# Performance work log

Measured on AMD Instinct MI355X. Metric: run time of the kernel, lower is better.

## Reference

```python
import jax, jax.numpy as jnp
import numpy as np
from jax import lax

B, S, H, SS, DS = 512, 200, 128, 2, 2  # batch, seq_len, hidden, static_size, dynamic_size

def _xavier(k, shape):
    fan_in, fan_out = shape[-1], shape[0]
    lim = float(np.sqrt(6.0 / (fan_in + fan_out)))
    return jax.random.uniform(k, shape, jnp.float32, -lim, lim)

def setup_inputs() -> dict:
    key = jax.random.key(0)
    ks = jax.random.split(key, 20)
    return {
        "static":  jax.random.uniform(ks[0], (B, SS, S), jnp.float32),
        "dynamic": jax.random.uniform(ks[1], (B, DS, S), jnp.float32),
        # Encoder: 1x1 Conv1d weights stored as [H, C] (kernel dim squeezed)
        "sW": _xavier(ks[2], (H, SS)),  "sb": jnp.zeros((H,), jnp.float32),
        "dW": _xavier(ks[3], (H, DS)),  "db": jnp.zeros((H,), jnp.float32),
        # Decoder learned initial output / hidden
        "x0": _xavier(ks[4], (1, SS)),  "h0": _xavier(ks[5], (1, H)),
        # Decoder input embedding Linear(SS -> H)
        "Wemb": _xavier(ks[6], (H, SS)), "bemb": jnp.zeros((H,), jnp.float32),
        # GRU (1 layer): torch layout [3H, H] gates ordered (r, z, n)
        "Wih": _xavier(ks[7], (3 * H, H)), "Whh": _xavier(ks[8], (3 * H, H)),
        "bih": jnp.zeros((3 * H,), jnp.float32), "bhh": jnp.zeros((3 * H,), jnp.float32),
        # Attention: v [H], W [H, 3H]
        "Wa": _xavier(ks[9], (H, 3 * H)), "va": _xavier(ks[10], (1, H))[0],
        # Decoder pointer head: v [H], W [H, 2H]
        "Wd": _xavier(ks[11], (H, 2 * H)), "vd": _xavier(ks[12], (1, H))[0],
    }

def _decode(static, dynamic, sW, sb, dW, db, x0, h0, Wemb, bemb,
            Wih, Whh, bih, bhh, Wa, va, Wd, vd):
    # Encoder: 1x1 convs == per-node linear maps  -> [B, H, S]
    static_enc  = jnp.einsum('hc,bcs->bhs', sW, static)  + sb[None, :, None]
    dynamic_enc = jnp.einsum('hc,bcs->bhs', dW, dynamic) + db[None, :, None]

    keys = jax.random.split(jax.random.key(42), S)  # one sample key per decode step
    static_sg = lax.stop_gradient(static)           # mirrors static.data gather in torch

    def step(carry, key):
        last_out, h = carry                              # [B,SS], [B,H]
        emb = last_out @ Wemb.T + bemb                   # [B,H]
        # GRU cell (torch gate order r, z, n)
        gi = emb @ Wih.T + bih                           # [B,3H]
        gh = h @ Whh.T + bhh
        r = jax.nn.sigmoid(gi[:, :H] + gh[:, :H])
        z = jax.nn.sigmoid(gi[:, H:2 * H] + gh[:, H:2 * H])
        n = jnp.tanh(gi[:, 2 * H:] + r * gh[:, 2 * H:])
        h_new = (1.0 - z) * n + z * h                    # [B,H]
        # Additive attention over nodes (vectorized over batch)
        hid = jnp.broadcast_to(h_new[:, :, None], (B, H, S))
        energy = jnp.concatenate([static_enc, dynamic_enc, hid], axis=1)   # [B,3H,S]
        attn = jax.nn.softmax(
            jnp.einsum('h,bhs->bs', va, jnp.tanh(jnp.einsum('hk,bks->bhs', Wa, energy))),
            axis=1)                                      # [B,S]
        context = jnp.einsum('bs,bhs->bh', attn, static_enc)               # [B,H]
        ctx = jnp.concatenate(
            [static_enc, jnp.broadcast_to(context[:, :, None], (B, H, S))], axis=1)  # [B,2H,S]
        logits = jnp.einsum('h,bhs->bs', vd,
                            jnp.tanh(jnp.einsum('hk,bks->bhs', Wd, ctx)))  # [B,S]
        # mask is all ones (mask_fn=None) -> log(mask)=0
        probs = jax.nn.softmax(logits, axis=1)
        idx = jax.random.categorical(key, logits, axis=1)                  # [B] int
        next_out = jnp.take_along_axis(static_sg, idx[:, None, None], axis=2)[:, :, 0]  # [B,SS]
        chosen_p = jnp.take_along_axis(probs, idx[:, None], axis=1)[:, 0]  # [B]
        return (next_out, h_new), (idx, chosen_p)

    init = (jnp.broadcast_to(x0, (B, SS)), jnp.broadcast_to(h0, (B, H)))
    _, (idx_seq, prob_seq) = lax.scan(step, init, keys)
    return idx_seq.T, prob_seq.T                          # [B,S] each

def reference(static, dynamic, sW, sb, dW, db, x0, h0, Wemb, bemb,
              Wih, Whh, bih, bhh, Wa, va, Wd, vd):
    return _decode(static, dynamic, sW, sb, dW, db, x0, h0, Wemb, bemb,
                   Wih, Whh, bih, bhh, Wa, va, Wd, vd)
```

## Files before the change

kernel.cpp:

```cpp
#include <hip/hip_runtime.h>
#include <stdint.h>
#include <math.h>

#define NB 512
#define NS 200
#define NH 128
#define NH3 384
#define NT 1024
#define NWAVE 16

#define IDX4(h) ((h) + (((h) >> 6) << 2))
#define IDX1(h) ((h) + (((h) >> 6) << 4))

__device__ __forceinline__ float xla_tanhf(float x) {
  float cx = fminf(fmaxf(x, -9.0f), 9.0f);
  float x2 = __fmul_rn(cx, cx);
  float p = -2.76076847742355e-16f;
  p = __fadd_rn(__fmul_rn(x2, p), 2.00018790482477e-13f);
  p = __fadd_rn(__fmul_rn(x2, p), -8.60467152213735e-11f);
  p = __fadd_rn(__fmul_rn(x2, p), 5.12229709037114e-08f);
  p = __fadd_rn(__fmul_rn(x2, p), 1.48572235717979e-05f);
  p = __fadd_rn(__fmul_rn(x2, p), 6.37261928875436e-04f);
  p = __fadd_rn(__fmul_rn(x2, p), 4.89352455891786e-03f);
  p = __fmul_rn(cx, p);
  float q = 1.19825839466702e-06f;
  q = __fadd_rn(__fmul_rn(x2, q), 1.18534705686654e-04f);
  q = __fadd_rn(__fmul_rn(x2, q), 2.26843463243900e-03f);
  q = __fadd_rn(__fmul_rn(x2, q), 4.89352518554385e-03f);
  float r = __fdiv_rn(p, q);
  return (fabsf(x) < 0.0004f) ? x : r;
}

__device__ __forceinline__ float xla_sigmoidf(float x) {
  return __fadd_rn(0.5f, __fmul_rn(0.5f, xla_tanhf(__fmul_rn(0.5f, x))));
}

__device__ __forceinline__ uint32_t rotl32(uint32_t v, int r) {
  return (v << r) | (v >> (32 - r));
}
__device__ __forceinline__ void threefry2x32(uint32_t k0, uint32_t k1,
                                             uint32_t x0, uint32_t x1,
                                             uint32_t& o0, uint32_t& o1) {
  uint32_t k2 = k0 ^ k1 ^ 0x1BD11BDAu;
  x0 += k0; x1 += k1;
  #define TFR(r) { x0 += x1; x1 = rotl32(x1, r); x1 ^= x0; }
  TFR(13) TFR(15) TFR(26) TFR(6)
  x0 += k1; x1 += k2 + 1u;
  TFR(17) TFR(29) TFR(16) TFR(24)
  x0 += k2; x1 += k0 + 2u;
  TFR(13) TFR(15) TFR(26) TFR(6)
  x0 += k0; x1 += k1 + 3u;
  TFR(17) TFR(29) TFR(16) TFR(24)
  x0 += k1; x1 += k2 + 4u;
  TFR(13) TFR(15) TFR(26) TFR(6)
  x0 += k2; x1 += k0 + 5u;
  #undef TFR
  o0 = x0; o1 = x1;
}

__device__ __forceinline__ float bits_to_gumbel(uint32_t bits) {
  const float kTiny = 1.1754943508222875e-38f;
  float f = __fsub_rn(__uint_as_float((bits >> 9) | 0x3F800000u), 1.0f);
  float u = __fadd_rn(__fmul_rn(f, __fsub_rn(1.0f, kTiny)), kTiny);
  u = fmaxf(kTiny, u);
  return -logf(-logf(u));
}

__global__ __launch_bounds__(NT, 4) void k_decode(
    const float* __restrict__ stat, const float* __restrict__ dyn,
    const float* __restrict__ sW,   const float* __restrict__ sb,
    const float* __restrict__ dW,   const float* __restrict__ db,
    const float* __restrict__ x0,   const float* __restrict__ h0,
    const float* __restrict__ Wemb, const float* __restrict__ bemb,
    const float* __restrict__ Wih,  const float* __restrict__ Whh,
    const float* __restrict__ bih,  const float* __restrict__ bhh,
    const float* __restrict__ Wa,   const float* __restrict__ va,
    const float* __restrict__ Wd,   const float* __restrict__ vd,
    float* __restrict__ out) {

  __shared__ __align__(16) float st0A[NS], st1A[NS], dy0A[NS], dy1A[NS];
  __shared__ __align__(16) float st0B[NS], st1B[NS], dy0B[NS], dy1B[NS];
  __shared__ float4 AF4p[132];
  __shared__ float4 DFSp[132];
  __shared__ float4 CW4[NH];
  __shared__ float  vaP[144];
  __shared__ float  Ht2A[144], Ht2B[144];
  __shared__ float  ct2A[144], ct2B[144];
  __shared__ float  AcL[NH];
  __shared__ float WembL[2*NH], bembL[NH];
  __shared__ float bihL[NH3], bhhL[NH3];
  __shared__ __align__(16) float embA[NH], embB[NH], hA[NH], hB[NH];
  __shared__ float giA[NH3], ghA[NH3], giB[NH3], ghB[NH3];
  __shared__ float ex2A[NS], ex2B[NS], gumA[NS], gumB[NS];
  __shared__ uint32_t keysL[2*NS];
  __shared__ float xpA[2], xpB[2];
  __shared__ float SvL[2];
  __shared__ float part[NWAVE][8];
  __shared__ int   partI[NWAVE];

  const int t = threadIdx.x;
  const int bA = blockIdx.x;
  const int bB = blockIdx.x + 256;
  const int w = t >> 6;
  const bool rB = (t >= 512);
  const int tr = rB ? (t - 512) : t;
  const int s = tr >> 1;
  const int h0i = (tr & 1) * 64;
  const int b4 = h0i + ((h0i >> 6) << 2);
  const int b1 = h0i + ((h0i >> 6) << 4);
  const bool act = (tr < 2*NS);

  if (t < NS) {
    st0A[t] = stat[(size_t)bA*2*NS + t];
    st1A[t] = stat[(size_t)bA*2*NS + NS + t];
    dy0A[t] = dyn[(size_t)bA*2*NS + t];
    dy1A[t] = dyn[(size_t)bA*2*NS + NS + t];
    uint32_t q0, q1;
    threefry2x32(0u, 42u, 0u, (uint32_t)t, q0, q1);
    keysL[2*t] = q0; keysL[2*t + 1] = q1;
  } else if (t >= 256 && t < 256 + NS) {
    int si = t - 256;
    st0B[si] = stat[(size_t)bB*2*NS + si];
    st1B[si] = stat[(size_t)bB*2*NS + NS + si];
    dy0B[si] = dyn[(size_t)bB*2*NS + si];
    dy1B[si] = dyn[(size_t)bB*2*NS + NS + si];
  }
  if (t >= 512 && t < 512 + NH) {
    int h = t - 512;
    const float* war = Wa + (size_t)h * NH3;
    float as0 = 0.f, as1 = 0.f, ad0 = 0.f, ad1 = 0.f, ac = 0.f;
    for (int k = 0; k < NH; ++k) {
      as0 = fmaf(war[k],     sW[k*2+0], as0);
      as1 = fmaf(war[k],     sW[k*2+1], as1);
      ad0 = fmaf(war[NH+k],  dW[k*2+0], ad0);
      ad1 = fmaf(war[NH+k],  dW[k*2+1], ad1);
      ac  = fmaf(war[k],     sb[k],     ac);
    }
    for (int k = 0; k < NH; ++k) ac = fmaf(war[NH+k], db[k], ac);
    AF4p[IDX4(h)] = make_float4(2.f*as0, 2.f*as1, 2.f*ad0, 2.f*ad1);
    vaP[IDX1(h)] = va[h];
    AcL[h] = ac;

    const float* wdr = Wd + (size_t)h * 256;
    float ds0 = 0.f, ds1 = 0.f, dc = 0.f, c0 = 0.f, c1 = 0.f, cb = 0.f;
    for (int k = 0; k < NH; ++k) {
      ds0 = fmaf(wdr[k],    sW[k*2+0], ds0);
      ds1 = fmaf(wdr[k],    sW[k*2+1], ds1);
      dc  = fmaf(wdr[k],    sb[k],     dc);
      c0  = fmaf(wdr[NH+k], sW[k*2+0], c0);
      c1  = fmaf(wdr[NH+k], sW[k*2+1], c1);
      cb  = fmaf(wdr[NH+k], sb[k],     cb);
    }
    DFSp[IDX4(h)] = make_float4(2.f*ds0, 2.f*ds1, vd[h], 0.f);
    CW4[h] = make_float4(2.f*c0, 2.f*c1, 2.f*cb, 2.f*dc);

    bembL[h] = bemb[h];
    WembL[2*h]   = Wemb[2*h];
    WembL[2*h+1] = Wemb[2*h+1];
    hA[h] = h0[h];
    hB[h] = h0[h];
  }
  for (int i = t; i < NH3; i += NT) { bihL[i] = bih[i]; bhhL[i] = bhh[i]; }
  if (t == 0) {
    xpA[0] = x0[0]; xpA[1] = x0[1];
    xpB[0] = x0[0]; xpB[1] = x0[1];
    float sva = 0.f, svd = 0.f;
    for (int h = 0; h < NH; ++h) { sva = __fadd_rn(sva, va[h]); svd = __fadd_rn(svd, vd[h]); }
    SvL[0] = sva; SvL[1] = svd;
  }
  __syncthreads();

  float s0r = 0.f, s1r = 0.f, d0r = 0.f, d1r = 0.f;
  if (act) {
    if (!rB) { s0r = st0A[s]; s1r = st1A[s]; d0r = dy0A[s]; d1r = dy1A[s]; }
    else     { s0r = st0B[s]; s1r = st1B[s]; d0r = dy0B[s]; d1r = dy1B[s]; }
  }
  const float svaR = SvL[0], svdR = SvL[1];
  const float* HtX = rB ? Ht2B : Ht2A;
  const float* ctX = rB ? ct2B : ct2A;
  const float* gumX = rB ? gumB : gumA;

  for (int step = 0; step < NS; ++step) {
    if (t < NH) {
      float e = fmaf(xpA[1], WembL[t*2+1], __fmul_rn(xpA[0], WembL[t*2+0]));
      embA[t] = __fadd_rn(e, bembL[t]);
    } else if (t < 2*NH) {
      int h = t - NH;
      float e = fmaf(xpB[1], WembL[h*2+1], __fmul_rn(xpB[0], WembL[h*2+0]));
      embB[h] = __fadd_rn(e, bembL[h]);
    } else if (t < 2*NH + 2*NS) {
      int gi = t - 2*NH;
      uint32_t k0 = keysL[2*step], k1 = keysL[2*step + 1];
      uint32_t q0, q1;
      if (gi < NS) {
        threefry2x32(k0, k1, 0u, (uint32_t)(bA*NS + gi), q0, q1);
        gumA[gi] = bits_to_gumbel(q0 ^ q1);
      } else {
        int si = gi - NS;
        threefry2x32(k0, k1, 0u, (uint32_t)(bB*NS + si), q0, q1);
        gumB[si] = bits_to_gumbel(q0 ^ q1);
      }
    }
    __syncthreads();

    if (t < 2*NH3) {
      const bool isWih = (t < NH3);
      const float4* wp = isWih
          ? (const float4*)(Wih + (size_t)t * NH)
          : (const float4*)(Whh + (size_t)(t - NH3) * NH);
      const float4* opA = isWih ? (const float4*)embA : (const float4*)hA;
      const float4* opB = isWih ? (const float4*)embB : (const float4*)hB;
      float aA = 0.f, aB = 0.f;
      #pragma unroll 8
      for (int k4 = 0; k4 < 32; ++k4) {
        float4 c = wp[k4];
        float4 vA = opA[k4], vB = opB[k4];
        aA = fmaf(c.x, vA.x, aA); aA = fmaf(c.y, vA.y, aA);
        aA = fmaf(c.z, vA.z, aA); aA = fmaf(c.w, vA.w, aA);
        aB = fmaf(c.x, vB.x, aB); aB = fmaf(c.y, vB.y, aB);
        aB = fmaf(c.z, vB.z, aB); aB = fmaf(c.w, vB.w, aB);
      }
      if (isWih) {
        giA[t] = __fadd_rn(aA, bihL[t]);
        giB[t] = __fadd_rn(aB, bihL[t]);
      } else {
        int row = t - NH3;
        ghA[row] = __fadd_rn(aA, bhhL[row]);
        ghB[row] = __fadd_rn(aB, bhhL[row]);
      }
    }
    __syncthreads();

    if (t < NH) {
      float r = xla_sigmoidf(__fadd_rn(giA[t],      ghA[t]));
      float z = xla_sigmoidf(__fadd_rn(giA[t+NH],   ghA[t+NH]));
      float n = xla_tanhf(__fadd_rn(giA[t+2*NH], __fmul_rn(r, ghA[t+2*NH])));
      float hv = hA[t];
      hA[t] = __fadd_rn(__fmul_rn(__fsub_rn(1.0f, z), n), __fmul_rn(z, hv));
    } else if (t < 2*NH) {
      int h = t - NH;
      float r = xla_sigmoidf(__fadd_rn(giB[h],      ghB[h]));
      float z = xla_sigmoidf(__fadd_rn(giB[h+NH],   ghB[h+NH]));
      float n = xla_tanhf(__fadd_rn(giB[h+2*NH], __fmul_rn(r, ghB[h+2*NH])));
      float hv = hB[h];
      hB[h] = __fadd_rn(__fmul_rn(__fsub_rn(1.0f, z), n), __fmul_rn(z, hv));
    }
    __syncthreads();

    if (t < NH) {
      const float4* war = (const float4*)(Wa + (size_t)t*NH3 + 2*NH);
      const float4* hn4 = (const float4*)hA;
      float acc = 0.f;
      #pragma unroll 8
      for (int k4 = 0; k4 < 32; ++k4) {
        float4 a = war[k4], hv = hn4[k4];
        acc = fmaf(a.x, hv.x, acc); acc = fmaf(a.y, hv.y, acc);
        acc = fmaf(a.z, hv.z, acc); acc = fmaf(a.w, hv.w, acc);
      }
      Ht2A[IDX1(t)] = __fmul_rn(2.0f, __fadd_rn(acc, AcL[t]));
    } else if (t < 2*NH) {
      int h = t - NH;
      const float4* war = (const float4*)(Wa + (size_t)h*NH3 + 2*NH);
      const float4* hn4 = (const float4*)hB;
      float acc = 0.f;
      #pragma unroll 8
      for (int k4 = 0; k4 < 32; ++k4) {
        float4 a = war[k4], hv = hn4[k4];
        acc = fmaf(a.x, hv.x, acc); acc = fmaf(a.y, hv.y, acc);
        acc = fmaf(a.z, hv.z, acc); acc = fmaf(a.w, hv.w, acc);
      }
      Ht2B[IDX1(h)] = __fmul_rn(2.0f, __fadd_rn(acc, AcL[h]));
    }
    __syncthreads();

    float accE = 0.f;
    if (act) {
      #pragma unroll 4
      for (int j = 0; j < 64; ++j) {
        float4 af = AF4p[b4 + j];
        float e2 = fmaf(af.x, s0r, HtX[b1 + j]);
        e2 = fmaf(af.y, s1r, e2);
        e2 = fmaf(af.z, d0r, e2);
        e2 = fmaf(af.w, d1r, e2);
        float r = __builtin_amdgcn_rcpf(__fadd_rn(__expf(e2), 1.0f));
        accE = fmaf(vaP[b1 + j], r, accE);
      }
    }
    float accSum = __fadd_rn(accE, __shfl_xor(accE, 1));
    float sc = act ? fmaf(-2.0f, accSum, svaR) : 0.f;

    float exv = act ? __expf(sc) : 0.f;
    {
      float sm = exv;
      float c0 = __fmul_rn(exv, s0r);
      float c1 = __fmul_rn(exv, s1r);
      #pragma unroll
      for (int mm = 2; mm < 64; mm <<= 1) {
        sm = __fadd_rn(sm, __shfl_xor(sm, mm));
        c0 = __fadd_rn(c0, __shfl_xor(c0, mm));
        c1 = __fadd_rn(c1, __shfl_xor(c1, mm));
      }
      if ((t & 63) == 0) { part[w][0] = sm; part[w][1] = c0; part[w][2] = c1; }
    }
    __syncthreads();

    if (t < 2*NH) {
      int h = t & (NH - 1);
      int base = (t < NH) ? 0 : 8;
      float sume = part[base][0], r0 = part[base][1], r1 = part[base][2];
      #pragma unroll
      for (int ww = 1; ww < 8; ++ww) {
        sume = __fadd_rn(sume, part[base + ww][0]);
        r0   = __fadd_rn(r0,   part[base + ww][1]);
        r1   = __fadd_rn(r1,   part[base + ww][2]);
      }
      r0 = __fdiv_rn(r0, sume); r1 = __fdiv_rn(r1, sume);
      float4 cw = CW4[h];
      float ct2 = fmaf(r0, cw.x, fmaf(r1, cw.y, cw.z));
      if (t < NH) ct2A[IDX1(h)] = __fadd_rn(cw.w, ct2);
      else        ct2B[IDX1(h)] = __fadd_rn(cw.w, ct2);
    }
    __syncthreads();

    float accD = 0.f;
    if (act) {
      #pragma unroll 4
      for (int j = 0; j < 64; ++j) {
        float4 df = DFSp[b4 + j];
        float d2 = fmaf(df.x, s0r, ctX[b1 + j]);
        d2 = fmaf(df.y, s1r, d2);
        float r = __builtin_amdgcn_rcpf(__fadd_rn(__expf(d2), 1.0f));
        accD = fmaf(df.z, r, accD);
      }
    }
    float accDS = __fadd_rn(accD, __shfl_xor(accD, 1));
    float sc2 = act ? fmaf(-2.0f, accDS, svdR) : 0.f;

    float e2v = act ? __expf(sc2) : 0.f;
    if (act && (tr & 1) == 0) { if (!rB) ex2A[s] = e2v; else ex2B[s] = e2v; }
    {
      float gv = -INFINITY;
      int gidx = 1 << 20;
      if (act) {
        gv = __fadd_rn(gumX[s], sc2);
        gidx = s;
      }
      float sm = e2v;
      #pragma unroll
      for (int mm = 2; mm < 64; mm <<= 1) {
        sm = __fadd_rn(sm, __shfl_xor(sm, mm));
        float ov = __shfl_xor(gv, mm); int oi = __shfl_xor(gidx, mm);
        if (ov > gv || (ov == gv && oi < gidx)) { gv = ov; gidx = oi; }
      }
      if ((t & 63) == 0) { part[w][3] = sm; part[w][4] = gv; partI[w] = gidx; }
    }
    __syncthreads();

    if (t == 0) {
      float bv = part[0][4]; int bi = partI[0];
      float sume2 = part[0][3];
      #pragma unroll
      for (int ww = 1; ww < 8; ++ww) {
        float vv = part[ww][4]; int ii = partI[ww];
        if (vv > bv || (vv == bv && ii < bi)) { bv = vv; bi = ii; }
        sume2 = __fadd_rn(sume2, part[ww][3]);
      }
      out[(size_t)bA*NS + step] = (float)bi;
      out[(size_t)NB*NS + (size_t)bA*NS + step] = __fdiv_rn(ex2A[bi], sume2);
      xpA[0] = st0A[bi]; xpA[1] = st1A[bi];
    } else if (t == 512) {
      float bv = part[8][4]; int bi = partI[8];
      float sume2 = part[8][3];
      #pragma unroll
      for (int ww = 9; ww < 16; ++ww) {
        float vv = part[ww][4]; int ii = partI[ww];
        if (vv > bv || (vv == bv && ii < bi)) { bv = vv; bi = ii; }
        sume2 = __fadd_rn(sume2, part[ww][3]);
      }
      out[(size_t)bB*NS + step] = (float)bi;
      out[(size_t)NB*NS + (size_t)bB*NS + step] = __fdiv_rn(ex2B[bi], sume2);
      xpB[0] = st0B[bi]; xpB[1] = st1B[bi];
    }
    __syncthreads();
  }
}

extern "C" void kernel_launch(void* const* d_in, const int* in_sizes, int n_in,
                              void* d_out, int out_size, void* d_ws, size_t ws_size,
                              hipStream_t stream) {
  (void)in_sizes; (void)n_in; (void)out_size; (void)d_ws; (void)ws_size;
  const float* stat = (const float*)d_in[0];
  const float* dyn  = (const float*)d_in[1];
  const float* sW   = (const float*)d_in[2];
  const float* sb   = (const float*)d_in[3];
  const float* dW   = (const float*)d_in[4];
  const float* db   = (const float*)d_in[5];
  const float* x0   = (const float*)d_in[6];
  const float* h0   = (const float*)d_in[7];
  const float* Wemb = (const float*)d_in[8];
  const float* bemb = (const float*)d_in[9];
  const float* Wih  = (const float*)d_in[10];
  const float* Whh  = (const float*)d_in[11];
  const float* bih  = (const float*)d_in[12];
  const float* bhh  = (const float*)d_in[13];
  const float* Wa   = (const float*)d_in[14];
  const float* va   = (const float*)d_in[15];
  const float* Wd   = (const float*)d_in[16];
  const float* vd   = (const float*)d_in[17];
  float* out = (float*)d_out;

  k_decode<<<NB/2, NT, 0, stream>>>(stat, dyn, sW, sb, dW, db, x0, h0,
                                    Wemb, bemb, Wih, Whh, bih, bhh,
                                    Wa, va, Wd, vd, out);
}
```

Baseline: 5.487 ms.

## Fuse embedding and Gumbel prep into step tail, use exp2 with split accumulators

Removes one block-wide barrier per decode step. Each step's tail phase now computes the next step's embedding directly from the chosen index, and threads 624 and up generate the next step's Gumbel noise there, so the shared xp buffers are dropped. The precomputed attention and pointer weights are prescaled by 2/ln2, which lets the sigmoid-like terms use exp2f instead of __expf. The inner loops are unrolled by two with separate accumulators to shorten dependency chains. Splitting the accumulators changes the summation order and rounding slightly, and the first step's noise and embedding are now computed before the loop.

```diff
diff --git a/kernel.cpp b/kernel.cpp
--- a/kernel.cpp
+++ b/kernel.cpp
@@ -8,6 +8,8 @@
 #define NH3 384
 #define NT 1024
 #define NWAVE 16
+
+#define SC2 2.8853900817779268f
 
 #define IDX4(h) ((h) + (((h) >> 6) << 2))
 #define IDX1(h) ((h) + (((h) >> 6) << 4))
@@ -93,7 +95,6 @@
   __shared__ float giA[NH3], ghA[NH3], giB[NH3], ghB[NH3];
   __shared__ float ex2A[NS], ex2B[NS], gumA[NS], gumB[NS];
   __shared__ uint32_t keysL[2*NS];
-  __shared__ float xpA[2], xpB[2];
   __shared__ float SvL[2];
   __shared__ float part[NWAVE][8];
   __shared__ int   partI[NWAVE];
@@ -137,7 +138,7 @@
       ac  = fmaf(war[k],     sb[k],     ac);
     }
     for (int k = 0; k < NH; ++k) ac = fmaf(war[NH+k], db[k], ac);
-    AF4p[IDX4(h)] = make_float4(2.f*as0, 2.f*as1, 2.f*ad0, 2.f*ad1);
+    AF4p[IDX4(h)] = make_float4(SC2*as0, SC2*as1, SC2*ad0, SC2*ad1);
     vaP[IDX1(h)] = va[h];
     AcL[h] = ac;
 
@@ -151,8 +152,8 @@
       c1  = fmaf(wdr[NH+k], sW[k*2+1], c1);
       cb  = fmaf(wdr[NH+k], sb[k],     cb);
     }
-    DFSp[IDX4(h)] = make_float4(2.f*ds0, 2.f*ds1, vd[h], 0.f);
-    CW4[h] = make_float4(2.f*c0, 2.f*c1, 2.f*cb, 2.f*dc);
+    DFSp[IDX4(h)] = make_float4(SC2*ds0, SC2*ds1, vd[h], 0.f);
+    CW4[h] = make_float4(SC2*c0, SC2*c1, SC2*cb, SC2*dc);
 
     bembL[h] = bemb[h];
     WembL[2*h]   = Wemb[2*h];
@@ -162,14 +163,31 @@
   }
   for (int i = t; i < NH3; i += NT) { bihL[i] = bih[i]; bhhL[i] = bhh[i]; }
   if (t == 0) {
-    xpA[0] = x0[0]; xpA[1] = x0[1];
-    xpB[0] = x0[0]; xpB[1] = x0[1];
     float sva = 0.f, svd = 0.f;
     for (int h = 0; h < NH; ++h) { sva = __fadd_rn(sva, va[h]); svd = __fadd_rn(svd, vd[h]); }
     SvL[0] = sva; SvL[1] = svd;
   }
   __syncthreads();
 
+  if (t < NH) {
+    float e = fmaf(x0[1], WembL[t*2+1], __fmul_rn(x0[0], WembL[t*2+0]));
+    embA[t] = __fadd_rn(e, bembL[t]);
+  } else if (t < 2*NH) {
+    int h = t - NH;
+    float e = fmaf(x0[1], WembL[h*2+1], __fmul_rn(x0[0], WembL[h*2+0]));
+    embB[h] = __fadd_rn(e, bembL[h]);
+  } else if (t >= 624) {
+    int gi = t - 624;
+    uint32_t q0, q1;
+    if (gi < NS) {
+      threefry2x32(keysL[0], keysL[1], 0u, (uint32_t)(bA*NS + gi), q0, q1);
+      gumA[gi] = bits_to_gumbel(q0 ^ q1);
+    } else {
+      int si = gi - NS;
+      threefry2x32(keysL[0], keysL[1], 0u, (uint32_t)(bB*NS + si), q0, q1);
+      gumB[si] = bits_to_gumbel(q0 ^ q1);
+    }
+  }
   float s0r = 0.f, s1r = 0.f, d0r = 0.f, d1r = 0.f;
   if (act) {
     if (!rB) { s0r = st0A[s]; s1r = st1A[s]; d0r = dy0A[s]; d1r = dy1A[s]; }
@@ -179,30 +197,9 @@
   const float* HtX = rB ? Ht2B : Ht2A;
   const float* ctX = rB ? ct2B : ct2A;
   const float* gumX = rB ? gumB : gumA;
+  __syncthreads();
 
   for (int step = 0; step < NS; ++step) {
-    if (t < NH) {
-      float e = fmaf(xpA[1], WembL[t*2+1], __fmul_rn(xpA[0], WembL[t*2+0]));
-      embA[t] = __fadd_rn(e, bembL[t]);
-    } else if (t < 2*NH) {
-      int h = t - NH;
-      float e = fmaf(xpB[1], WembL[h*2+1], __fmul_rn(xpB[0], WembL[h*2+0]));
-      embB[h] = __fadd_rn(e, bembL[h]);
-    } else if (t < 2*NH + 2*NS) {
-      int gi = t - 2*NH;
-      uint32_t k0 = keysL[2*step], k1 = keysL[2*step + 1];
-      uint32_t q0, q1;
-      if (gi < NS) {
-        threefry2x32(k0, k1, 0u, (uint32_t)(bA*NS + gi), q0, q1);
-        gumA[gi] = bits_to_gumbel(q0 ^ q1);
-      } else {
-        int si = gi - NS;
-        threefry2x32(k0, k1, 0u, (uint32_t)(bB*NS + si), q0, q1);
-        gumB[si] = bits_to_gumbel(q0 ^ q1);
-      }
-    }
-    __syncthreads();
-
     if (t < 2*NH3) {
       const bool isWih = (t < NH3);
       const float4* wp = isWih
@@ -257,7 +254,7 @@
         acc = fmaf(a.x, hv.x, acc); acc = fmaf(a.y, hv.y, acc);
         acc = fmaf(a.z, hv.z, acc); acc = fmaf(a.w, hv.w, acc);
       }
-      Ht2A[IDX1(t)] = __fmul_rn(2.0f, __fadd_rn(acc, AcL[t]));
+      Ht2A[IDX1(t)] = __fmul_rn(SC2, __fadd_rn(acc, AcL[t]));
     } else if (t < 2*NH) {
       int h = t - NH;
       const float4* war = (const float4*)(Wa + (size_t)h*NH3 + 2*NH);
@@ -269,23 +266,31 @@
         acc = fmaf(a.x, hv.x, acc); acc = fmaf(a.y, hv.y, acc);
         acc = fmaf(a.z, hv.z, acc); acc = fmaf(a.w, hv.w, acc);
       }
-      Ht2B[IDX1(h)] = __fmul_rn(2.0f, __fadd_rn(acc, AcL[h]));
-    }
-    __syncthreads();
-
-    float accE = 0.f;
+      Ht2B[IDX1(h)] = __fmul_rn(SC2, __fadd_rn(acc, AcL[h]));
+    }
+    __syncthreads();
+
+    float accE0 = 0.f, accE1 = 0.f;
     if (act) {
       #pragma unroll 4
-      for (int j = 0; j < 64; ++j) {
-        float4 af = AF4p[b4 + j];
-        float e2 = fmaf(af.x, s0r, HtX[b1 + j]);
-        e2 = fmaf(af.y, s1r, e2);
-        e2 = fmaf(af.z, d0r, e2);
-        e2 = fmaf(af.w, d1r, e2);
-        float r = __builtin_amdgcn_rcpf(__fadd_rn(__expf(e2), 1.0f));
-        accE = fmaf(vaP[b1 + j], r, accE);
-      }
-    }
+      for (int j = 0; j < 64; j += 2) {
+        float4 af0 = AF4p[b4 + j];
+        float e0 = fmaf(af0.x, s0r, HtX[b1 + j]);
+        e0 = fmaf(af0.y, s1r, e0);
+        e0 = fmaf(af0.z, d0r, e0);
+        e0 = fmaf(af0.w, d1r, e0);
+        float r0v = __builtin_amdgcn_rcpf(__fadd_rn(exp2f(e0), 1.0f));
+        accE0 = fmaf(vaP[b1 + j], r0v, accE0);
+        float4 af1 = AF4p[b4 + j + 1];
+        float e1 = fmaf(af1.x, s0r, HtX[b1 + j + 1]);
+        e1 = fmaf(af1.y, s1r, e1);
+        e1 = fmaf(af1.z, d0r, e1);
+        e1 = fmaf(af1.w, d1r, e1);
+        float r1v = __builtin_amdgcn_rcpf(__fadd_rn(exp2f(e1), 1.0f));
+        accE1 = fmaf(vaP[b1 + j + 1], r1v, accE1);
+      }
+    }
+    float accE = __fadd_rn(accE0, accE1);
     float accSum = __fadd_rn(accE, __shfl_xor(accE, 1));
     float sc = act ? fmaf(-2.0f, accSum, svaR) : 0.f;
 
@@ -322,17 +327,23 @@
     }
     __syncthreads();
 
-    float accD = 0.f;
+    float accD0 = 0.f, accD1 = 0.f;
     if (act) {
       #pragma unroll 4
-      for (int j = 0; j < 64; ++j) {
-        float4 df = DFSp[b4 + j];
-        float d2 = fmaf(df.x, s0r, ctX[b1 + j]);
-        d2 = fmaf(df.y, s1r, d2);
-        float r = __builtin_amdgcn_rcpf(__fadd_rn(__expf(d2), 1.0f));
-        accD = fmaf(df.z, r, accD);
-      }
-    }
+      for (int j = 0; j < 64; j += 2) {
+        float4 df0 = DFSp[b4 + j];
+        float d0 = fmaf(df0.x, s0r, ctX[b1 + j]);
+        d0 = fmaf(df0.y, s1r, d0);
+        float r0v = __builtin_amdgcn_rcpf(__fadd_rn(exp2f(d0), 1.0f));
+        accD0 = fmaf(df0.z, r0v, accD0);
+        float4 df1 = DFSp[b4 + j + 1];
+        float d1 = fmaf(df1.x, s0r, ctX[b1 + j + 1]);
+        d1 = fmaf(df1.y, s1r, d1);
+        float r1v = __builtin_amdgcn_rcpf(__fadd_rn(exp2f(d1), 1.0f));
+        accD1 = fmaf(df1.z, r1v, accD1);
+      }
+    }
+    float accD = __fadd_rn(accD0, accD1);
     float accDS = __fadd_rn(accD, __shfl_xor(accD, 1));
     float sc2 = act ? fmaf(-2.0f, accDS, svdR) : 0.f;
 
@@ -356,30 +367,46 @@
     }
     __syncthreads();
 
-    if (t == 0) {
-      float bv = part[0][4]; int bi = partI[0];
-      float sume2 = part[0][3];
+    if (t < 2*NH) {
+      int base = (t < NH) ? 0 : 8;
+      float bv = part[base][4]; int bi = partI[base];
+      float sume2 = part[base][3];
       #pragma unroll
       for (int ww = 1; ww < 8; ++ww) {
-        float vv = part[ww][4]; int ii = partI[ww];
+        float vv = part[base + ww][4]; int ii = partI[base + ww];
         if (vv > bv || (vv == bv && ii < bi)) { bv = vv; bi = ii; }
-        sume2 = __fadd_rn(sume2, part[ww][3]);
-      }
-      out[(size_t)bA*NS + step] = (float)bi;
-      out[(size_t)NB*NS + (size_t)bA*NS + step] = __fdiv_rn(ex2A[bi], sume2);
-      xpA[0] = st0A[bi]; xpA[1] = st1A[bi];
-    } else if (t == 512) {
-      float bv = part[8][4]; int bi = partI[8];
-      float sume2 = part[8][3];
-      #pragma unroll
-      for (int ww = 9; ww < 16; ++ww) {
-        float vv = part[ww][4]; int ii = partI[ww];
-        if (vv > bv || (vv == bv && ii < bi)) { bv = vv; bi = ii; }
-        sume2 = __fadd_rn(sume2, part[ww][3]);
-      }
-      out[(size_t)bB*NS + step] = (float)bi;
-      out[(size_t)NB*NS + (size_t)bB*NS + step] = __fdiv_rn(ex2B[bi], sume2);
-      xpB[0] = st0B[bi]; xpB[1] = st1B[bi];
+        sume2 = __fadd_rn(sume2, part[base + ww][3]);
+      }
+      if (t == 0) {
+        out[(size_t)bA*NS + step] = (float)bi;
+        out[(size_t)NB*NS + (size_t)bA*NS + step] = __fdiv_rn(ex2A[bi], sume2);
+      } else if (t == NH) {
+        out[(size_t)bB*NS + step] = (float)bi;
+        out[(size_t)NB*NS + (size_t)bB*NS + step] = __fdiv_rn(ex2B[bi], sume2);
+      }
+      if (t < NH) {
+        float xa = st0A[bi], xb = st1A[bi];
+        float e = fmaf(xb, WembL[t*2+1], __fmul_rn(xa, WembL[t*2+0]));
+        embA[t] = __fadd_rn(e, bembL[t]);
+      } else {
+        int h = t - NH;
+        float xa = st0B[bi], xb = st1B[bi];
+        float e = fmaf(xb, WembL[h*2+1], __fmul_rn(xa, WembL[h*2+0]));
+        embB[h] = __fadd_rn(e, bembL[h]);
+      }
+    } else if (t >= 624) {
+      int nstep = (step + 1 < NS) ? (step + 1) : step;
+      int gi = t - 624;
+      uint32_t k0 = keysL[2*nstep], k1 = keysL[2*nstep + 1];
+      uint32_t q0, q1;
+      if (gi < NS) {
+        threefry2x32(k0, k1, 0u, (uint32_t)(bA*NS + gi), q0, q1);
+        gumA[gi] = bits_to_gumbel(q0 ^ q1);
+      } else {
+        int si = gi - NS;
+        threefry2x32(k0, k1, 0u, (uint32_t)(bB*NS + si), q0, q1);
+        gumB[si] = bits_to_gumbel(q0 ^ q1);
+      }
     }
     __syncthreads();
   }
```

Measured after the change: 5.921 ms. +7.9%, slower.
